# Kernel optimization log

Measured on AMD Instinct MI355X. Metric: run time of the kernel, lower is better.

## Reference

```python
import jax, jax.numpy as jnp
import numpy as np

DIM = 768
NUM_HEADS = 12
MAX_DIST = 32


def _build_relative_index(max_dist):
    # Faithful port of the torch buffer construction (pure numpy, static).
    ii, jj = np.meshgrid(np.arange(max_dist), np.arange(max_dist), indexing='ij')
    coords_flat = np.stack([ii.reshape(-1), jj.reshape(-1)], axis=0)  # [2, max_dist^2]
    rel = coords_flat[:, :, None] - coords_flat[:, None, :]          # [2, L, L]
    rel = rel.transpose(1, 2, 0) + (max_dist - 1)
    rel_index = rel[:, :, 0] * (2 * max_dist - 1) + rel[:, :, 1]
    return jnp.asarray(rel_index, dtype=jnp.int32)                   # [L, L]


def setup_inputs() -> dict:
    key = jax.random.key(0)
    k_x, k_qkv, k_proj, k_pb, k_bt = jax.random.split(key, 5)
    B, N, C = 8, 1024, DIM
    std = 0.02
    x = jax.random.normal(k_x, (B, N, C), dtype=jnp.float32)
    qkv_w = jax.random.normal(k_qkv, (C, 3 * C), dtype=jnp.float32) * std  # Linear(dim, 3*dim, bias=False)
    proj_w = jax.random.normal(k_proj, (C, C), dtype=jnp.float32) * std
    proj_b = jax.random.normal(k_pb, (C,), dtype=jnp.float32) * std
    bias_table = jax.random.normal(k_bt, ((2 * MAX_DIST - 1) ** 2, NUM_HEADS), dtype=jnp.float32) * std
    rel_index = _build_relative_index(MAX_DIST)
    return {"x": x, "qkv_w": qkv_w, "proj_w": proj_w, "proj_b": proj_b,
            "bias_table": bias_table, "rel_index": rel_index}


def reference(x, qkv_w, proj_w, proj_b, bias_table, rel_index):
    B, N, C = x.shape
    H = NUM_HEADS
    hd = C // H
    scale = hd ** -0.5
    qkv = (x @ qkv_w).reshape(B, N, 3, H, hd)
    q, k, v = qkv[:, :, 0], qkv[:, :, 1], qkv[:, :, 2]          # [B, N, H, hd]
    attn = jnp.einsum('bnhd,bmhd->bhnm', q, k) * scale           # [B, H, N, N]
    # gathered relative position bias, added per head before softmax
    rel_bias = bias_table[rel_index[:N, :N].reshape(-1)]         # [N*N, H]
    rel_bias = rel_bias.reshape(N, N, H).transpose(2, 0, 1)      # [H, N, N]
    attn = jax.nn.softmax(attn + rel_bias[None], axis=-1)
    out = jnp.einsum('bhnm,bmhd->bnhd', attn, v).reshape(B, N, C)
    return out @ proj_w + proj_b
```

## Files before the change

### kernel.cpp

```cpp
#include <hip/hip_runtime.h>
#include <hip/hip_bf16.h>
#include <stdint.h>

typedef unsigned short u16;
typedef __attribute__((ext_vector_type(8))) short short8;
typedef __attribute__((ext_vector_type(8))) __bf16 bf16x8;
typedef __attribute__((ext_vector_type(4))) float floatx4;

#define DIMC 768
#define NH   12
#define HD   64
#define NB   8
#define SEQ  1024
#define MROWS (NB*SEQ)
#define BTAB_N 47628
#define PB_N   768

__device__ __forceinline__ float bf2f(u16 u){ return __uint_as_float(((uint32_t)u)<<16); }
__device__ __forceinline__ u16 f2bf(float f){
  uint32_t u = __float_as_uint(f);
  u += 0x7fffu + ((u>>16)&1u);
  return (u16)(u>>16);
}
__device__ __forceinline__ floatx4 mfma16(short8 a, short8 b, floatx4 c){
  return __builtin_amdgcn_mfma_f32_16x16x32_bf16(
      __builtin_bit_cast(bf16x8, a), __builtin_bit_cast(bf16x8, b), c, 0, 0, 0);
}

__global__ __launch_bounds__(256) void detect_dtype(
    const u16* __restrict__ x, int* __restrict__ flag)
{
  __shared__ int cnt[256];
  int c = 0;
  for (int i = threadIdx.x; i < 2048; i += 256) {
    int e = (x[i] >> 7) & 0xFF;
    c += (e >= 0x8E);
  }
  cnt[threadIdx.x] = c;
  __syncthreads();
  for (int s = 128; s > 0; s >>= 1) {
    if ((int)threadIdx.x < s) cnt[threadIdx.x] += cnt[threadIdx.x + s];
    __syncthreads();
  }
  if (threadIdx.x == 0) *flag = (cnt[0] > 16) ? 1 : 0;
}

__global__ __launch_bounds__(256) void convert_x(
    const void* __restrict__ in, u16* __restrict__ outp,
    const int* __restrict__ flag, int n4)
{
  int idx = blockIdx.x * 256 + threadIdx.x;
  if (idx >= n4) return;
  ushort4 o;
  if (*flag) {
    const float4 v = ((const float4*)in)[idx];
    o.x = f2bf(v.x); o.y = f2bf(v.y); o.z = f2bf(v.z); o.w = f2bf(v.w);
  } else {
    o = ((const ushort4*)in)[idx];
  }
  ((ushort4*)outp)[idx] = o;
}

__global__ __launch_bounds__(256) void convert_small(
    const void* __restrict__ btab, const void* __restrict__ pb,
    u16* __restrict__ btabB, u16* __restrict__ pbB, const int* __restrict__ flag)
{
  int f = *flag;
  int idx = blockIdx.x * 256 + threadIdx.x;
  if (idx < BTAB_N) {
    btabB[idx] = f ? f2bf(((const float*)btab)[idx]) : ((const u16*)btab)[idx];
  } else if (idx < BTAB_N + PB_N) {
    int j = idx - BTAB_N;
    pbB[j] = f ? f2bf(((const float*)pb)[j]) : ((const u16*)pb)[j];
  }
}

__global__ __launch_bounds__(256) void transpose_any(
    const void* __restrict__ in, u16* __restrict__ out, int R, int C,
    const int* __restrict__ flag)
{
  __shared__ __align__(16) u16 t[64][65];
  const int f = *flag;
  const size_t bo = (size_t)blockIdx.z * R * C;
  const int r0 = blockIdx.y * 64, c0 = blockIdx.x * 64;
  const int tx = threadIdx.x & 63, ty = threadIdx.x >> 6;
  #pragma unroll
  for (int i = ty; i < 64; i += 4) {
    size_t src = bo + (size_t)(r0 + i) * C + c0 + tx;
    t[i][tx] = f ? f2bf(((const float*)in)[src]) : ((const u16*)in)[src];
  }
  __syncthreads();
  #pragma unroll
  for (int i = ty; i < 64; i += 4)
    out[bo + (size_t)(c0 + i) * R + r0 + tx] = t[tx][i];
}

__global__ __launch_bounds__(256) void build_bias(
    const int* __restrict__ rel, const u16* __restrict__ table, u16* __restrict__ biasM)
{
  const int t = blockIdx.x * 256 + threadIdx.x;
  const int idx = rel[t];
  const u16* row = table + idx * NH;
  #pragma unroll
  for (int h = 0; h < NH; ++h)
    biasM[(size_t)h * (SEQ * SEQ) + t] = row[h];
}

template<int MODE>
__global__ __launch_bounds__(256) void gemm_bt(
    const u16* __restrict__ A, const u16* __restrict__ Bt,
    int M, int N, int K,
    u16* __restrict__ Qb, u16* __restrict__ Kb, u16* __restrict__ Vt,
    float* __restrict__ Out, const u16* __restrict__ bias)
{
  __shared__ __align__(16) u16 As[128][72];
  __shared__ __align__(16) u16 Bs[128][72];
  const int m0 = blockIdx.x * 128, n0 = blockIdx.y * 128;
  const int tid = threadIdx.x;
  const int wave = tid >> 6, lane = tid & 63;
  const int wx = wave & 1, wy = wave >> 1;
  const int r = lane & 15, quad = lane >> 4;

  const floatx4 zf = {0.f, 0.f, 0.f, 0.f};
  floatx4 acc[4][4];
  #pragma unroll
  for (int i = 0; i < 4; ++i)
    #pragma unroll
    for (int j = 0; j < 4; ++j) acc[i][j] = zf;

  for (int kt = 0; kt < K; kt += 64) {
    __syncthreads();
    #pragma unroll
    for (int i = 0; i < 4; ++i) {
      int c = tid + i * 256;
      int row = c >> 3, ch = (c & 7) * 8;
      *(int4*)&As[row][ch] = *(const int4*)&A[(size_t)(m0 + row) * K + kt + ch];
      *(int4*)&Bs[row][ch] = *(const int4*)&Bt[(size_t)(n0 + row) * K + kt + ch];
    }
    __syncthreads();
    #pragma unroll
    for (int ks = 0; ks < 64; ks += 32) {
      short8 a[4], b[4];
      #pragma unroll
      for (int i = 0; i < 4; ++i) a[i] = *(const short8*)&As[wy * 64 + i * 16 + r][ks + quad * 8];
      #pragma unroll
      for (int j = 0; j < 4; ++j) b[j] = *(const short8*)&Bs[wx * 64 + j * 16 + r][ks + quad * 8];
      #pragma unroll
      for (int i = 0; i < 4; ++i)
        #pragma unroll
        for (int j = 0; j < 4; ++j)
          acc[i][j] = mfma16(a[i], b[j], acc[i][j]);
    }
  }

  #pragma unroll
  for (int i = 0; i < 4; ++i)
    #pragma unroll
    for (int j = 0; j < 4; ++j)
      #pragma unroll
      for (int g = 0; g < 4; ++g) {
        int gm = m0 + wy * 64 + i * 16 + quad * 4 + g;
        int gn = n0 + wx * 64 + j * 16 + r;
        float v = acc[i][j][g];
        if (MODE == 0) {
          int three = gn / DIMC;
          int hn = gn - three * DIMC;
          int h = hn >> 6, d = hn & 63;
          int b_ = gm >> 10, n = gm & 1023;
          int bh = b_ * NH + h;
          if (three == 0)      Qb[(((size_t)bh) * SEQ + n) * HD + d] = f2bf(v * 0.125f);
          else if (three == 1) Kb[(((size_t)bh) * SEQ + n) * HD + d] = f2bf(v);
          else                 Vt[(((size_t)bh) * HD + d) * SEQ + n] = f2bf(v);
        } else {
          Out[(size_t)gm * N + gn] = v + bf2f(bias[gn]);
        }
      }
}

template<int USEB>
__global__ __launch_bounds__(256) void attention(
    const u16* __restrict__ Qb, const u16* __restrict__ Kb, const u16* __restrict__ Vt,
    const u16* __restrict__ biasB, u16* __restrict__ Ob)
{
  __shared__ __align__(16) u16 Qs[128][72];
  __shared__ __align__(16) u16 Ks[64][72];
  __shared__ __align__(16) u16 Vs[64][72];
  __shared__ __align__(16) u16 Ps[4][32][72];

  const int bh = blockIdx.x;
  const int h = bh % NH, b_ = bh / NH;
  const int q0 = blockIdx.y * 128;
  const int tid = threadIdx.x;
  const int wave = tid >> 6, lane = tid & 63;
  const int r = lane & 15, quad = lane >> 4;

  const u16* Qp = Qb + (size_t)bh * SEQ * HD;
  const u16* Kp = Kb + (size_t)bh * SEQ * HD;
  const u16* Vp = Vt + (size_t)bh * HD * SEQ;
  const u16* Bp = USEB ? (biasB + (size_t)h * SEQ * SEQ) : biasB;

  #pragma unroll
  for (int i = 0; i < 4; ++i) {
    int c = tid + i * 256;
    int row = c >> 3, ch = (c & 7) * 8;
    *(int4*)&Qs[row][ch] = *(const int4*)&Qp[(size_t)(q0 + row) * HD + ch];
  }

  const floatx4 zf = {0.f, 0.f, 0.f, 0.f};
  floatx4 o[2][4];
  float mrow[2][4], lrow[2][4];
  #pragma unroll
  for (int i = 0; i < 2; ++i) {
    #pragma unroll
    for (int dj = 0; dj < 4; ++dj) o[i][dj] = zf;
    #pragma unroll
    for (int g = 0; g < 4; ++g) { mrow[i][g] = -1e30f; lrow[i][g] = 0.f; }
  }

  for (int kt = 0; kt < 16; ++kt) {
    __syncthreads();
    #pragma unroll
    for (int i = 0; i < 2; ++i) {
      int c = tid + i * 256;
      int row = c >> 3, ch = (c & 7) * 8;
      *(int4*)&Ks[row][ch] = *(const int4*)&Kp[(size_t)(kt * 64 + row) * HD + ch];
      *(int4*)&Vs[row][ch] = *(const int4*)&Vp[(size_t)row * SEQ + kt * 64 + ch];
    }
    __syncthreads();

    floatx4 s[2][4];
    #pragma unroll
    for (int i = 0; i < 2; ++i)
      #pragma unroll
      for (int j = 0; j < 4; ++j) s[i][j] = zf;

    #pragma unroll
    for (int ks = 0; ks < 64; ks += 32) {
      short8 aq[2], bk[4];
      #pragma unroll
      for (int i = 0; i < 2; ++i) aq[i] = *(const short8*)&Qs[wave * 32 + i * 16 + r][ks + quad * 8];
      #pragma unroll
      for (int j = 0; j < 4; ++j) bk[j] = *(const short8*)&Ks[j * 16 + r][ks + quad * 8];
      #pragma unroll
      for (int i = 0; i < 2; ++i)
        #pragma unroll
        for (int j = 0; j < 4; ++j)
          s[i][j] = mfma16(aq[i], bk[j], s[i][j]);
    }

    #pragma unroll
    for (int i = 0; i < 2; ++i)
      #pragma unroll
      for (int j = 0; j < 4; ++j)
        #pragma unroll
        for (int g = 0; g < 4; ++g) {
          const int q = q0 + wave * 32 + i * 16 + quad * 4 + g;
          const int k = kt * 64 + j * 16 + r;
          if (USEB) {
            s[i][j][g] += bf2f(Bp[(size_t)q * SEQ + k]);
          } else {
            const int idx = ((q >> 5) - (k >> 5) + 31) * 63 + ((q & 31) - (k & 31) + 31);
            s[i][j][g] += bf2f(Bp[idx * NH + h]);
          }
        }

    float tmax[2][4], rs[2][4];
    #pragma unroll
    for (int i = 0; i < 2; ++i)
      #pragma unroll
      for (int g = 0; g < 4; ++g) {
        float m = s[i][0][g];
        #pragma unroll
        for (int j = 1; j < 4; ++j) m = fmaxf(m, s[i][j][g]);
        tmax[i][g] = m;
      }
    #pragma unroll
    for (int off = 1; off < 16; off <<= 1)
      #pragma unroll
      for (int i = 0; i < 2; ++i)
        #pragma unroll
        for (int g = 0; g < 4; ++g)
          tmax[i][g] = fmaxf(tmax[i][g], __shfl_xor(tmax[i][g], off, 64));

    #pragma unroll
    for (int i = 0; i < 2; ++i)
      #pragma unroll
      for (int g = 0; g < 4; ++g) {
        float mn = fmaxf(mrow[i][g], tmax[i][g]);
        float al = __expf(mrow[i][g] - mn);
        mrow[i][g] = mn;
        lrow[i][g] *= al;
        #pragma unroll
        for (int dj = 0; dj < 4; ++dj) o[i][dj][g] *= al;
        rs[i][g] = 0.f;
      }

    #pragma unroll
    for (int i = 0; i < 2; ++i)
      #pragma unroll
      for (int j = 0; j < 4; ++j)
        #pragma unroll
        for (int g = 0; g < 4; ++g) {
          float pv = __expf(s[i][j][g] - mrow[i][g]);
          s[i][j][g] = pv;
          rs[i][g] += pv;
        }
    #pragma unroll
    for (int off = 1; off < 16; off <<= 1)
      #pragma unroll
      for (int i = 0; i < 2; ++i)
        #pragma unroll
        for (int g = 0; g < 4; ++g)
          rs[i][g] += __shfl_xor(rs[i][g], off, 64);
    #pragma unroll
    for (int i = 0; i < 2; ++i)
      #pragma unroll
      for (int g = 0; g < 4; ++g) lrow[i][g] += rs[i][g];

    #pragma unroll
    for (int i = 0; i < 2; ++i)
      #pragma unroll
      for (int j = 0; j < 4; ++j)
        #pragma unroll
        for (int g = 0; g < 4; ++g)
          Ps[wave][i * 16 + quad * 4 + g][j * 16 + r] = f2bf(s[i][j][g]);
    __syncthreads();

    #pragma unroll
    for (int kk = 0; kk < 2; ++kk) {
      short8 ap[2], bv[4];
      #pragma unroll
      for (int i = 0; i < 2; ++i) ap[i] = *(const short8*)&Ps[wave][i * 16 + r][kk * 32 + quad * 8];
      #pragma unroll
      for (int dj = 0; dj < 4; ++dj) bv[dj] = *(const short8*)&Vs[dj * 16 + r][kk * 32 + quad * 8];
      #pragma unroll
      for (int i = 0; i < 2; ++i)
        #pragma unroll
        for (int dj = 0; dj < 4; ++dj)
          o[i][dj] = mfma16(ap[i], bv[dj], o[i][dj]);
    }
  }

  #pragma unroll
  for (int i = 0; i < 2; ++i)
    #pragma unroll
    for (int g = 0; g < 4; ++g) {
      float inv = 1.0f / lrow[i][g];
      int q = q0 + wave * 32 + i * 16 + quad * 4 + g;
      #pragma unroll
      for (int dj = 0; dj < 4; ++dj) {
        int d = dj * 16 + r;
        Ob[((size_t)(b_ * SEQ + q)) * DIMC + h * HD + d] = f2bf(o[i][dj][g] * inv);
      }
    }
}

extern "C" void kernel_launch(void* const* d_in, const int* in_sizes, int n_in,
                              void* d_out, int out_size, void* d_ws, size_t ws_size,
                              hipStream_t stream)
{
  (void)in_sizes; (void)n_in; (void)out_size;
  const void* x_raw  = d_in[0];
  const void* qkv_w  = d_in[1];
  const void* proj_w = d_in[2];
  const void* proj_b = d_in[3];
  const void* btab   = d_in[4];
  const int*  rel    = (const int*)d_in[5];
  float* out = (float*)d_out;

  const size_t SZ_FLAG = 256;
  const size_t SZ_XB   = (size_t)MROWS * DIMC * 2;
  const size_t SZ_BTAB = (BTAB_N * 2 + 255) & ~(size_t)255;
  const size_t SZ_PB   = (PB_N * 2 + 255) & ~(size_t)255;
  const size_t SZ_WQT  = (size_t)3 * DIMC * DIMC * 2;
  const size_t SZ_WPT  = (size_t)DIMC * DIMC * 2;
  const size_t SZ_T    = (size_t)NB * NH * SEQ * HD * 2;
  const size_t SZ_BM   = (size_t)NH * SEQ * SEQ * 2;
  const size_t NEED_FULL = SZ_FLAG + SZ_XB + SZ_BTAB + SZ_PB + SZ_WQT + SZ_WPT
                         + 3 * SZ_T + SZ_BM;

  char* p = (char*)d_ws;
  int* flag  = (int*)p;  p += SZ_FLAG;
  u16* xB    = (u16*)p;  p += SZ_XB;
  u16* btabB = (u16*)p;  p += SZ_BTAB;
  u16* pbB   = (u16*)p;  p += SZ_PB;
  u16* wqT   = (u16*)p;  p += SZ_WQT;
  u16* wpT   = (u16*)p;  p += SZ_WPT;
  u16* Qb    = (u16*)p;  p += SZ_T;
  u16* Kb    = (u16*)p;  p += SZ_T;
  u16* Vt    = (u16*)p;  p += SZ_T;
  u16* biasM = (u16*)p;

  const bool useBiasM = (ws_size >= NEED_FULL);
  const int n4 = MROWS * DIMC / 4;

  detect_dtype<<<1, 256, 0, stream>>>((const u16*)x_raw, flag);
  convert_x<<<(n4 + 255) / 256, 256, 0, stream>>>(x_raw, xB, flag, n4);
  convert_small<<<(BTAB_N + PB_N + 255) / 256, 256, 0, stream>>>(btab, proj_b, btabB, pbB, flag);
  transpose_any<<<dim3(3 * DIMC / 64, DIMC / 64, 1), 256, 0, stream>>>(qkv_w, wqT, DIMC, 3 * DIMC, flag);
  transpose_any<<<dim3(DIMC / 64, DIMC / 64, 1), 256, 0, stream>>>(proj_w, wpT, DIMC, DIMC, flag);
  gemm_bt<0><<<dim3(MROWS / 128, 3 * DIMC / 128), 256, 0, stream>>>(
      xB, wqT, MROWS, 3 * DIMC, DIMC, Qb, Kb, Vt, nullptr, nullptr);
  if (useBiasM) {
    build_bias<<<SEQ * SEQ / 256, 256, 0, stream>>>(rel, btabB, biasM);
    attention<1><<<dim3(NB * NH, SEQ / 128), 256, 0, stream>>>(Qb, Kb, Vt, biasM, xB);
  } else {
    attention<0><<<dim3(NB * NH, SEQ / 128), 256, 0, stream>>>(Qb, Kb, Vt, btabB, xB);
  }
  gemm_bt<1><<<dim3(MROWS / 128, DIMC / 128), 256, 0, stream>>>(
      xB, wpT, MROWS, DIMC, DIMC, nullptr, nullptr, nullptr, out, pbB);
}
```

Before: 320.2 us.

## Compute transposed scores so P stays in registers and drop LDS P round-trip

```diff
diff --git a/kernel.cpp b/kernel.cpp
--- a/kernel.cpp
+++ b/kernel.cpp
@@ -21,6 +21,9 @@
   uint32_t u = __float_as_uint(f);
   u += 0x7fffu + ((u>>16)&1u);
   return (u16)(u>>16);
+}
+__device__ __forceinline__ uint32_t pack2(float lo, float hi){
+  return (uint32_t)f2bf(lo) | ((uint32_t)f2bf(hi) << 16);
 }
 __device__ __forceinline__ floatx4 mfma16(short8 a, short8 b, floatx4 c){
   return __builtin_amdgcn_mfma_f32_16x16x32_bf16(
@@ -178,21 +181,22 @@
 }
 
 template<int USEB>
-__global__ __launch_bounds__(256) void attention(
+__global__ __launch_bounds__(256, 4) void attention(
     const u16* __restrict__ Qb, const u16* __restrict__ Kb, const u16* __restrict__ Vt,
     const u16* __restrict__ biasB, u16* __restrict__ Ob)
 {
   __shared__ __align__(16) u16 Qs[128][72];
   __shared__ __align__(16) u16 Ks[64][72];
   __shared__ __align__(16) u16 Vs[64][72];
-  __shared__ __align__(16) u16 Ps[4][32][72];
 
   const int bh = blockIdx.x;
   const int h = bh % NH, b_ = bh / NH;
   const int q0 = blockIdx.y * 128;
   const int tid = threadIdx.x;
   const int wave = tid >> 6, lane = tid & 63;
-  const int r = lane & 15, quad = lane >> 4;
+  const int r15 = lane & 15, quad = lane >> 4;
+  const int upper = quad >> 1;
+  const int srcBase = r15 + 16 * ((quad & 1) * 2);
 
   const u16* Qp = Qb + (size_t)bh * SEQ * HD;
   const u16* Kp = Kb + (size_t)bh * SEQ * HD;
@@ -207,15 +211,12 @@
   }
 
   const floatx4 zf = {0.f, 0.f, 0.f, 0.f};
-  floatx4 o[2][4];
-  float mrow[2][4], lrow[2][4];
-  #pragma unroll
-  for (int i = 0; i < 2; ++i) {
-    #pragma unroll
-    for (int dj = 0; dj < 4; ++dj) o[i][dj] = zf;
-    #pragma unroll
-    for (int g = 0; g < 4; ++g) { mrow[i][g] = -1e30f; lrow[i][g] = 0.f; }
-  }
+  floatx4 o[4][2];
+  float mrow[2] = {-1e30f, -1e30f}, lrow[2] = {0.f, 0.f};
+  #pragma unroll
+  for (int Jm = 0; Jm < 4; ++Jm)
+    #pragma unroll
+    for (int i = 0; i < 2; ++i) o[Jm][i] = zf;
 
   for (int kt = 0; kt < 16; ++kt) {
     __syncthreads();
@@ -228,131 +229,120 @@
     }
     __syncthreads();
 
-    floatx4 s[2][4];
+    floatx4 sT[2][4];
     #pragma unroll
     for (int i = 0; i < 2; ++i)
       #pragma unroll
-      for (int j = 0; j < 4; ++j) s[i][j] = zf;
+      for (int Jk = 0; Jk < 4; ++Jk) sT[i][Jk] = zf;
 
     #pragma unroll
     for (int ks = 0; ks < 64; ks += 32) {
-      short8 aq[2], bk[4];
-      #pragma unroll
-      for (int i = 0; i < 2; ++i) aq[i] = *(const short8*)&Qs[wave * 32 + i * 16 + r][ks + quad * 8];
-      #pragma unroll
-      for (int j = 0; j < 4; ++j) bk[j] = *(const short8*)&Ks[j * 16 + r][ks + quad * 8];
+      short8 ak[4], bq[2];
+      #pragma unroll
+      for (int Jk = 0; Jk < 4; ++Jk) ak[Jk] = *(const short8*)&Ks[Jk * 16 + r15][ks + quad * 8];
+      #pragma unroll
+      for (int i = 0; i < 2; ++i)    bq[i]  = *(const short8*)&Qs[wave * 32 + i * 16 + r15][ks + quad * 8];
       #pragma unroll
       for (int i = 0; i < 2; ++i)
         #pragma unroll
-        for (int j = 0; j < 4; ++j)
-          s[i][j] = mfma16(aq[i], bk[j], s[i][j]);
-    }
-
-    #pragma unroll
-    for (int i = 0; i < 2; ++i)
-      #pragma unroll
-      for (int j = 0; j < 4; ++j)
-        #pragma unroll
-        for (int g = 0; g < 4; ++g) {
-          const int q = q0 + wave * 32 + i * 16 + quad * 4 + g;
-          const int k = kt * 64 + j * 16 + r;
-          if (USEB) {
-            s[i][j][g] += bf2f(Bp[(size_t)q * SEQ + k]);
-          } else {
+        for (int Jk = 0; Jk < 4; ++Jk)
+          sT[i][Jk] = mfma16(ak[Jk], bq[i], sT[i][Jk]);
+    }
+
+    uint32_t p2[2][4][2];
+    #pragma unroll
+    for (int i = 0; i < 2; ++i) {
+      const int q = q0 + wave * 32 + i * 16 + r15;
+      #pragma unroll
+      for (int Jk = 0; Jk < 4; ++Jk) {
+        const int kb = kt * 64 + Jk * 16 + quad * 4;
+        if (USEB) {
+          const ushort4 bv = *(const ushort4*)&Bp[(size_t)q * SEQ + kb];
+          sT[i][Jk][0] += bf2f(bv.x); sT[i][Jk][1] += bf2f(bv.y);
+          sT[i][Jk][2] += bf2f(bv.z); sT[i][Jk][3] += bf2f(bv.w);
+        } else {
+          #pragma unroll
+          for (int g = 0; g < 4; ++g) {
+            const int k = kb + g;
             const int idx = ((q >> 5) - (k >> 5) + 31) * 63 + ((q & 31) - (k & 31) + 31);
-            s[i][j][g] += bf2f(Bp[idx * NH + h]);
+            sT[i][Jk][g] += bf2f(Bp[idx * NH + h]);
           }
         }
-
-    float tmax[2][4], rs[2][4];
-    #pragma unroll
-    for (int i = 0; i < 2; ++i)
-      #pragma unroll
-      for (int g = 0; g < 4; ++g) {
-        float m = s[i][0][g];
-        #pragma unroll
-        for (int j = 1; j < 4; ++j) m = fmaxf(m, s[i][j][g]);
-        tmax[i][g] = m;
       }
-    #pragma unroll
-    for (int off = 1; off < 16; off <<= 1)
-      #pragma unroll
-      for (int i = 0; i < 2; ++i)
-        #pragma unroll
-        for (int g = 0; g < 4; ++g)
-          tmax[i][g] = fmaxf(tmax[i][g], __shfl_xor(tmax[i][g], off, 64));
-
-    #pragma unroll
-    for (int i = 0; i < 2; ++i)
-      #pragma unroll
-      for (int g = 0; g < 4; ++g) {
-        float mn = fmaxf(mrow[i][g], tmax[i][g]);
-        float al = __expf(mrow[i][g] - mn);
-        mrow[i][g] = mn;
-        lrow[i][g] *= al;
-        #pragma unroll
-        for (int dj = 0; dj < 4; ++dj) o[i][dj][g] *= al;
-        rs[i][g] = 0.f;
+      float m = sT[i][0][0];
+      #pragma unroll
+      for (int Jk = 0; Jk < 4; ++Jk)
+        #pragma unroll
+        for (int g = 0; g < 4; ++g) m = fmaxf(m, sT[i][Jk][g]);
+      m = fmaxf(m, __shfl_xor(m, 16, 64));
+      m = fmaxf(m, __shfl_xor(m, 32, 64));
+      const float mn = fmaxf(mrow[i], m);
+      const float al = __expf(mrow[i] - mn);
+      mrow[i] = mn;
+      float rs = 0.f;
+      #pragma unroll
+      for (int Jk = 0; Jk < 4; ++Jk)
+        #pragma unroll
+        for (int g = 0; g < 4; ++g) {
+          const float pv = __expf(sT[i][Jk][g] - mn);
+          sT[i][Jk][g] = pv;
+          rs += pv;
+        }
+      rs += __shfl_xor(rs, 16, 64);
+      rs += __shfl_xor(rs, 32, 64);
+      lrow[i] = lrow[i] * al + rs;
+      #pragma unroll
+      for (int Jm = 0; Jm < 4; ++Jm) {
+        o[Jm][i][0] *= al; o[Jm][i][1] *= al; o[Jm][i][2] *= al; o[Jm][i][3] *= al;
       }
-
-    #pragma unroll
-    for (int i = 0; i < 2; ++i)
-      #pragma unroll
-      for (int j = 0; j < 4; ++j)
-        #pragma unroll
-        for (int g = 0; g < 4; ++g) {
-          float pv = __expf(s[i][j][g] - mrow[i][g]);
-          s[i][j][g] = pv;
-          rs[i][g] += pv;
+      #pragma unroll
+      for (int J = 0; J < 4; ++J) {
+        p2[i][J][0] = pack2(sT[i][J][0], sT[i][J][1]);
+        p2[i][J][1] = pack2(sT[i][J][2], sT[i][J][3]);
+      }
+    }
+
+    #pragma unroll
+    for (int kk = 0; kk < 2; ++kk) {
+      short8 av[4];
+      #pragma unroll
+      for (int Jm = 0; Jm < 4; ++Jm)
+        av[Jm] = *(const short8*)&Vs[Jm * 16 + r15][kk * 32 + quad * 8];
+      #pragma unroll
+      for (int i = 0; i < 2; ++i) {
+        uint32_t w[4];
+        #pragma unroll
+        for (int hf = 0; hf < 2; ++hf) {
+          const int src = srcBase + 16 * hf;
+          const uint32_t lo0 = (uint32_t)__shfl((int)p2[i][2 * kk][0], src, 64);
+          const uint32_t hi0 = (uint32_t)__shfl((int)p2[i][2 * kk][1], src, 64);
+          const uint32_t lo1 = (uint32_t)__shfl((int)p2[i][2 * kk + 1][0], src, 64);
+          const uint32_t hi1 = (uint32_t)__shfl((int)p2[i][2 * kk + 1][1], src, 64);
+          w[2 * hf]     = upper ? lo1 : lo0;
+          w[2 * hf + 1] = upper ? hi1 : hi0;
         }
-    #pragma unroll
-    for (int off = 1; off < 16; off <<= 1)
-      #pragma unroll
-      for (int i = 0; i < 2; ++i)
-        #pragma unroll
-        for (int g = 0; g < 4; ++g)
-          rs[i][g] += __shfl_xor(rs[i][g], off, 64);
-    #pragma unroll
-    for (int i = 0; i < 2; ++i)
-      #pragma unroll
-      for (int g = 0; g < 4; ++g) lrow[i][g] += rs[i][g];
-
-    #pragma unroll
-    for (int i = 0; i < 2; ++i)
-      #pragma unroll
-      for (int j = 0; j < 4; ++j)
-        #pragma unroll
-        for (int g = 0; g < 4; ++g)
-          Ps[wave][i * 16 + quad * 4 + g][j * 16 + r] = f2bf(s[i][j][g]);
-    __syncthreads();
-
-    #pragma unroll
-    for (int kk = 0; kk < 2; ++kk) {
-      short8 ap[2], bv[4];
-      #pragma unroll
-      for (int i = 0; i < 2; ++i) ap[i] = *(const short8*)&Ps[wave][i * 16 + r][kk * 32 + quad * 8];
-      #pragma unroll
-      for (int dj = 0; dj < 4; ++dj) bv[dj] = *(const short8*)&Vs[dj * 16 + r][kk * 32 + quad * 8];
-      #pragma unroll
-      for (int i = 0; i < 2; ++i)
-        #pragma unroll
-        for (int dj = 0; dj < 4; ++dj)
-          o[i][dj] = mfma16(ap[i], bv[dj], o[i][dj]);
-    }
-  }
-
-  #pragma unroll
-  for (int i = 0; i < 2; ++i)
-    #pragma unroll
-    for (int g = 0; g < 4; ++g) {
-      float inv = 1.0f / lrow[i][g];
-      int q = q0 + wave * 32 + i * 16 + quad * 4 + g;
-      #pragma unroll
-      for (int dj = 0; dj < 4; ++dj) {
-        int d = dj * 16 + r;
-        Ob[((size_t)(b_ * SEQ + q)) * DIMC + h * HD + d] = f2bf(o[i][dj][g] * inv);
+        const short8 bp = __builtin_bit_cast(short8, *(uint4*)w);
+        #pragma unroll
+        for (int Jm = 0; Jm < 4; ++Jm)
+          o[Jm][i] = mfma16(av[Jm], bp, o[Jm][i]);
       }
     }
+  }
+
+  #pragma unroll
+  for (int i = 0; i < 2; ++i) {
+    const float inv = 1.0f / lrow[i];
+    const int q = q0 + wave * 32 + i * 16 + r15;
+    #pragma unroll
+    for (int Jm = 0; Jm < 4; ++Jm) {
+      ushort4 st;
+      st.x = f2bf(o[Jm][i][0] * inv);
+      st.y = f2bf(o[Jm][i][1] * inv);
+      st.z = f2bf(o[Jm][i][2] * inv);
+      st.w = f2bf(o[Jm][i][3] * inv);
+      *(ushort4*)&Ob[((size_t)(b_ * SEQ + q)) * DIMC + h * HD + Jm * 16 + quad * 4] = st;
+    }
+  }
 }
 
 extern "C" void kernel_launch(void* const* d_in, const int* in_sizes, int n_in,
```

Result: faster. 282.5 us (-11.8%).
